# Optimization experiments

Measured on AMD Instinct MI355X. Metric: run time of the kernel, lower is better.

The kernel has to match this reference:

```python
import jax, jax.numpy as jnp
import numpy as np
from jax import lax

DN = ('NCDHW', 'OIDHW', 'NCDHW')

def _conv(x, W, strides, padding):
    return lax.conv_general_dilated(x, W, strides, padding, dimension_numbers=DN)

def setup_inputs() -> dict:
    key = jax.random.key(0)
    ks = jax.random.split(key, 7)
    B, Cin, D, H, Wd = 1, 128, 41, 128, 128
    C = 64
    feat = jax.random.normal(ks[0], (B, Cin, D, H, Wd), jnp.float32)
    mask = jax.random.uniform(ks[1], (B, 1, D, H, Wd), jnp.float32)
    def w(k, co, ci, kd, kh, kw):
        fan_in = ci * kd * kh * kw
        return jax.random.normal(k, (co, ci, kd, kh, kw), jnp.float32) * (1.0 / np.sqrt(fan_in))
    return {
        'feat': feat,
        'mask': mask,
        'W_subm0': w(ks[2], C, Cin, 3, 3, 3),
        'W_down1': w(ks[3], C, C, 3, 1, 1),
        'W_subm1a': w(ks[4], C, C, 3, 3, 3),
        'W_subm1b': w(ks[5], C, C, 3, 3, 3),
        'W_down2': w(ks[6], C, C, 3, 1, 1),
    }

def reference(feat, mask, W_subm0, W_down1, W_subm1a, W_subm1b, W_down2):
    # generate_sparse: keep only voxels where mask > 0.5 (features outside are dropped)
    m = (mask > 0.5).astype(feat.dtype)  # [B,1,D,H,W] active-site indicator
    x = feat * m
    # SubMConv3d(128->64, k=3, same) : output only at active sites -> mask the dense conv
    x = jax.nn.relu(_conv(x, W_subm0, (1, 1, 1), 'SAME') * m)
    # SparseConv3d(64->64, k=(3,1,1), stride=(2,1,1), pad=0): dense strided conv is exact
    # since x is zero at inactive sites and .dense() zero-fills inactive outputs.
    x = jax.nn.relu(_conv(x, W_down1, (2, 1, 1), 'VALID'))
    # new active set: any active input voxel in the (3,1,1)/stride-(2,1,1) window
    m = lax.reduce_window(m, 0.0, lax.max, (1, 1, 3, 1, 1), (1, 1, 2, 1, 1), 'VALID')
    # two SubMConv3d(64->64, k=3, same) on the downsampled active set
    x = jax.nn.relu(_conv(x, W_subm1a, (1, 1, 1), 'SAME') * m)
    x = jax.nn.relu(_conv(x, W_subm1b, (1, 1, 1), 'SAME') * m)
    # second strided SparseConv3d + ReLU, then .dense()
    x = jax.nn.relu(_conv(x, W_down2, (2, 1, 1), 'VALID'))
    return x  # [B, 64, 9, 128, 128]
```

## Files before the change

### kernel.cpp

```cpp
#include <hip/hip_runtime.h>

typedef __attribute__((ext_vector_type(8))) _Float16 f16x8;
typedef __attribute__((ext_vector_type(4))) float f32x4;

#define NVOX0 (41L*16384)
#define NVOX1 (20L*16384)

#define OFF_X0 0L
#define SZ_X0  (NVOX0*128*2)
#define OFF_X2 0L
#define SZ_X2  (NVOX1*64*2)
#define OFF_X3 SZ_X2
#define OFF_X4 0L
#define OFF_X1 SZ_X0
#define SZ_X1  (NVOX0*64*2)
#define OFF_M1 (OFF_X1 + SZ_X1)
#define SZ_M1  (NVOX1*4)
#define OFF_W0 (OFF_M1 + SZ_M1)
#define SZ_W0  (27L*64*128*2)
#define OFF_W1 (OFF_W0 + SZ_W0)
#define SZ_W1  (3L*64*64*2)
#define OFF_W2 (OFF_W1 + SZ_W1)
#define SZ_W2  (27L*64*64*2)
#define OFF_W3 (OFF_W2 + SZ_W2)
#define SZ_W3  (27L*64*64*2)
#define OFF_W4 (OFF_W3 + SZ_W3)
#define SZ_W4  (3L*64*64*2)

__global__ void prep_w_frag(const float* __restrict__ w, _Float16* __restrict__ o,
                            int CIN, int NK, int T) {
    int i = blockIdx.x * 256 + threadIdx.x;
    int n = T * NK * 2048;
    if (i >= n) return;
    int e = i & 7;
    int lane = (i >> 3) & 63;
    int nt = (i >> 9) & 3;
    int rest = i >> 11;
    int kc = rest % NK;
    int t = rest / NK;
    int co = nt * 16 + (lane & 15);
    int ci = kc * 32 + (lane >> 4) * 8 + e;
    o[i] = (_Float16)w[((long)co * CIN + ci) * T + t];
}

__global__ void prep_w(const float* __restrict__ w, _Float16* __restrict__ o,
                       int CO, int CI, int T) {
    int i = blockIdx.x * 256 + threadIdx.x;
    int n = CO * CI * T;
    if (i >= n) return;
    int t  = i % T;
    int ci = (i / T) % CI;
    int co = i / (T * CI);
    o[((long)t * CO + co) * CI + ci] = (_Float16)w[i];
}

__global__ void prep_m1(const float* __restrict__ mask, float* __restrict__ m1) {
    int i = blockIdx.x * 256 + threadIdx.x;
    if (i >= (int)NVOX1) return;
    int d1 = i >> 14;
    int rr = i & 16383;
    const float* p = mask + ((long)(2 * d1) << 14) + rr;
    float mx = fmaxf(p[0], fmaxf(p[16384], p[32768]));
    m1[i] = (mx > 0.5f) ? 1.0f : 0.0f;
}

__global__ __launch_bounds__(256)
void prep_x0(const float* __restrict__ feat, const float* __restrict__ mask,
             _Float16* __restrict__ x0) {
    long v = (long)blockIdx.x * 256 + threadIdx.x;
    if (v >= NVOX0) return;
    float m = (mask[v] > 0.5f) ? 1.0f : 0.0f;
    const float* fp = feat + v;
    _Float16* op = x0 + v * 128;
    #pragma unroll 2
    for (int ci0 = 0; ci0 < 128; ci0 += 8) {
        f16x8 pk;
        #pragma unroll
        for (int k = 0; k < 8; ++k)
            pk[k] = (_Float16)(fp[(long)(ci0 + k) * NVOX0] * m);
        *(f16x8*)&op[ci0] = pk;
    }
}

template<int CIN>
__global__ __launch_bounds__(128)
void subm_conv(const _Float16* __restrict__ xin,
               const float* __restrict__ mrow,
               const _Float16* __restrict__ wf,
               _Float16* __restrict__ xout,
               int D) {
    constexpr int NCH = CIN / 8;
    constexpr int NK  = CIN / 32;
    __shared__ __align__(16) _Float16 lA[130 * CIN];

    const int bid = blockIdx.x;
    const int h = ((bid & 7) << 4) | ((bid >> 3) & 15);
    const int d = bid >> 7;
    const int tid = threadIdx.x;
    const int wh = tid >> 6;
    const int lane = tid & 63;
    const int q = lane >> 4;
    const int r = lane & 15;

    f32x4 acc[4][4];
    #pragma unroll
    for (int mt = 0; mt < 4; ++mt)
        #pragma unroll
        for (int nt = 0; nt < 4; ++nt) {
            acc[mt][nt][0] = 0.f; acc[mt][nt][1] = 0.f;
            acc[mt][nt][2] = 0.f; acc[mt][nt][3] = 0.f;
        }

    for (int kd = 0; kd < 3; ++kd) {
        int id = d + kd - 1;
        if ((unsigned)id >= (unsigned)D) continue;
        for (int kh = 0; kh < 3; ++kh) {
            int ih = h + kh - 1;
            if ((unsigned)ih >= 128u) continue;
            __syncthreads();
            if (tid < 2 * NCH) {
                int slot = (tid < NCH) ? 0 : 129;
                int j = tid & (NCH - 1);
                f16x8 z = {};
                *(f16x8*)&lA[slot * CIN + j * 8] = z;
            }
            {
                const _Float16* src = xin + (((long)id * 128 + ih) * 128) * CIN;
                #pragma unroll
                for (int k = 0; k < NCH; ++k) {
                    int c = tid + k * 128;
                    int v = c / NCH;
                    int j = c & (NCH - 1);
                    int slot = v + 1;
                    f16x8 val = *(const f16x8*)&src[c * 8];
                    *(f16x8*)&lA[slot * CIN + ((j ^ (slot & 7)) << 3)] = val;
                }
            }
            __syncthreads();
            #pragma unroll
            for (int kw = 0; kw < 3; ++kw) {
                const _Float16* wb = wf + (long)((kd * 3 + kh) * 3 + kw) * NK * 2048;
                #pragma unroll
                for (int kc = 0; kc < NK; ++kc) {
                    f16x8 bf[4], af[4];
                    #pragma unroll
                    for (int nt = 0; nt < 4; ++nt)
                        bf[nt] = *(const f16x8*)&wb[((kc * 4 + nt) * 64 + lane) * 8];
                    #pragma unroll
                    for (int mt = 0; mt < 4; ++mt) {
                        int vl = wh * 64 + mt * 16 + r + kw;
                        af[mt] = *(const f16x8*)&lA[vl * CIN +
                                   ((((kc << 2) + q) ^ (vl & 7)) << 3)];
                    }
                    #pragma unroll
                    for (int mt = 0; mt < 4; ++mt)
                        #pragma unroll
                        for (int nt = 0; nt < 4; ++nt)
                            acc[mt][nt] = __builtin_amdgcn_mfma_f32_16x16x32_f16(
                                af[mt], bf[nt], acc[mt][nt], 0, 0, 0);
                }
            }
        }
    }
    long ob = (((long)d * 128 + h) * 128) * 64;
    const float* mo = mrow + ((long)d * 128 + h) * 128;
    #pragma unroll
    for (int mt = 0; mt < 4; ++mt) {
        #pragma unroll
        for (int i = 0; i < 4; ++i) {
            int v = wh * 64 + mt * 16 + q * 4 + i;
            float m = (mo[v] > 0.5f) ? 1.0f : 0.0f;
            #pragma unroll
            for (int nt = 0; nt < 4; ++nt) {
                float val = acc[mt][nt][i];
                val = val > 0.f ? val : 0.f;
                xout[ob + (long)v * 64 + nt * 16 + r] = (_Float16)(val * m);
            }
        }
    }
}

__global__ __launch_bounds__(128)
void down1_kernel(const _Float16* __restrict__ xin,
                  const _Float16* __restrict__ wt,
                  _Float16* __restrict__ xout) {
    __shared__ __align__(16) _Float16 lB[3 * 64 * 72];
    const int bid = blockIdx.x;
    const int d1 = bid >> 7;
    const int h = bid & 127;
    const int tid = threadIdx.x;
    const int wv = tid >> 6;
    const int lane = tid & 63;
    const int q = lane >> 4;
    const int r = lane & 15;

    for (int c = tid; c < 3 * 64 * 8; c += 128) {
        int row = c >> 3;
        int part = c & 7;
        *(f16x8*)&lB[row * 72 + part * 8] = *(const f16x8*)&wt[row * 64 + part * 8];
    }
    __syncthreads();

    f32x4 acc[4][4];
    #pragma unroll
    for (int mt = 0; mt < 4; ++mt)
        #pragma unroll
        for (int nt = 0; nt < 4; ++nt) {
            acc[mt][nt][0] = 0.f; acc[mt][nt][1] = 0.f;
            acc[mt][nt][2] = 0.f; acc[mt][nt][3] = 0.f;
        }

    for (int kd = 0; kd < 3; ++kd) {
        long ib = (((long)(2 * d1 + kd) * 128 + h) * 128) * 64;
        #pragma unroll
        for (int kc = 0; kc < 2; ++kc) {
            f16x8 af[4], bf[4];
            #pragma unroll
            for (int mt = 0; mt < 4; ++mt)
                af[mt] = *(const f16x8*)&xin[ib + (long)(wv * 64 + mt * 16 + r) * 64 + kc * 32 + q * 8];
            #pragma unroll
            for (int nt = 0; nt < 4; ++nt)
                bf[nt] = *(const f16x8*)&lB[(kd * 64 + nt * 16 + r) * 72 + kc * 32 + q * 8];
            #pragma unroll
            for (int mt = 0; mt < 4; ++mt)
                #pragma unroll
                for (int nt = 0; nt < 4; ++nt)
                    acc[mt][nt] = __builtin_amdgcn_mfma_f32_16x16x32_f16(
                        af[mt], bf[nt], acc[mt][nt], 0, 0, 0);
        }
    }
    long ob = (((long)d1 * 128 + h) * 128) * 64;
    #pragma unroll
    for (int mt = 0; mt < 4; ++mt)
        #pragma unroll
        for (int i = 0; i < 4; ++i) {
            int v = wv * 64 + mt * 16 + q * 4 + i;
            #pragma unroll
            for (int nt = 0; nt < 4; ++nt) {
                float val = acc[mt][nt][i];
                xout[ob + (long)v * 64 + nt * 16 + r] = (_Float16)(val > 0.f ? val : 0.f);
            }
        }
}

__global__ __launch_bounds__(128)
void down2_kernel(const _Float16* __restrict__ xin,
                  const _Float16* __restrict__ wt,
                  float* __restrict__ out) {
    __shared__ __align__(16) _Float16 lB[3 * 64 * 72];
    const int bid = blockIdx.x;
    const int d2 = bid >> 7;
    const int h = bid & 127;
    const int tid = threadIdx.x;
    const int wv = tid >> 6;
    const int lane = tid & 63;
    const int q = lane >> 4;
    const int r = lane & 15;

    for (int c = tid; c < 3 * 64 * 8; c += 128) {
        int row = c >> 3;
        int part = c & 7;
        *(f16x8*)&lB[row * 72 + part * 8] = *(const f16x8*)&wt[row * 64 + part * 8];
    }
    __syncthreads();

    f32x4 acc[4][4];
    #pragma unroll
    for (int mt = 0; mt < 4; ++mt)
        #pragma unroll
        for (int nt = 0; nt < 4; ++nt) {
            acc[mt][nt][0] = 0.f; acc[mt][nt][1] = 0.f;
            acc[mt][nt][2] = 0.f; acc[mt][nt][3] = 0.f;
        }

    for (int kd = 0; kd < 3; ++kd) {
        long ib = (((long)(2 * d2 + kd) * 128 + h) * 128) * 64;
        #pragma unroll
        for (int kc = 0; kc < 2; ++kc) {
            f16x8 wfr[4], xf[4];
            #pragma unroll
            for (int mt = 0; mt < 4; ++mt)
                wfr[mt] = *(const f16x8*)&lB[(kd * 64 + mt * 16 + r) * 72 + kc * 32 + q * 8];
            #pragma unroll
            for (int nt = 0; nt < 4; ++nt)
                xf[nt] = *(const f16x8*)&xin[ib + (long)(wv * 64 + nt * 16 + r) * 64 + kc * 32 + q * 8];
            #pragma unroll
            for (int mt = 0; mt < 4; ++mt)
                #pragma unroll
                for (int nt = 0; nt < 4; ++nt)
                    acc[mt][nt] = __builtin_amdgcn_mfma_f32_16x16x32_f16(
                        wfr[mt], xf[nt], acc[mt][nt], 0, 0, 0);
        }
    }
    #pragma unroll
    for (int mt = 0; mt < 4; ++mt)
        #pragma unroll
        for (int i = 0; i < 4; ++i) {
            int co = mt * 16 + q * 4 + i;
            #pragma unroll
            for (int nt = 0; nt < 4; ++nt) {
                int v = wv * 64 + nt * 16 + r;
                float val = acc[mt][nt][i];
                out[((long)co * 9 + d2) * 16384 + h * 128 + v] = (val > 0.f ? val : 0.f);
            }
        }
}

extern "C" void kernel_launch(void* const* d_in, const int* in_sizes, int n_in,
                              void* d_out, int out_size, void* d_ws, size_t ws_size,
                              hipStream_t stream) {
    (void)in_sizes; (void)n_in; (void)out_size; (void)ws_size;
    const float* feat = (const float*)d_in[0];
    const float* mask = (const float*)d_in[1];
    const float* w0 = (const float*)d_in[2];
    const float* w1 = (const float*)d_in[3];
    const float* w2 = (const float*)d_in[4];
    const float* w3 = (const float*)d_in[5];
    const float* w4 = (const float*)d_in[6];

    char* ws = (char*)d_ws;
    _Float16* X0  = (_Float16*)(ws + OFF_X0);
    _Float16* X1  = (_Float16*)(ws + OFF_X1);
    _Float16* X2  = (_Float16*)(ws + OFF_X2);
    _Float16* X3  = (_Float16*)(ws + OFF_X3);
    _Float16* X4  = (_Float16*)(ws + OFF_X4);
    float*    M1  = (float*)(ws + OFF_M1);
    _Float16* W0f = (_Float16*)(ws + OFF_W0);
    _Float16* W1t = (_Float16*)(ws + OFF_W1);
    _Float16* W2f = (_Float16*)(ws + OFF_W2);
    _Float16* W3f = (_Float16*)(ws + OFF_W3);
    _Float16* W4t = (_Float16*)(ws + OFF_W4);

    prep_w_frag<<<(27*4*2048 + 255) / 256, 256, 0, stream>>>(w0, W0f, 128, 4, 27);
    prep_w_frag<<<(27*2*2048 + 255) / 256, 256, 0, stream>>>(w2, W2f, 64, 2, 27);
    prep_w_frag<<<(27*2*2048 + 255) / 256, 256, 0, stream>>>(w3, W3f, 64, 2, 27);
    prep_w<<<(3*64*64 + 255) / 256, 256, 0, stream>>>(w1, W1t, 64, 64, 3);
    prep_w<<<(3*64*64 + 255) / 256, 256, 0, stream>>>(w4, W4t, 64, 64, 3);
    prep_m1<<<((int)NVOX1 + 255) / 256, 256, 0, stream>>>(mask, M1);
    prep_x0<<<(int)(NVOX0 / 256), 256, 0, stream>>>(feat, mask, X0);

    subm_conv<128><<<41 * 128, 128, 0, stream>>>(X0, mask, W0f, X1, 41);
    down1_kernel<<<20 * 128, 128, 0, stream>>>(X1, W1t, X2);
    subm_conv<64><<<20 * 128, 128, 0, stream>>>(X2, M1, W2f, X3, 20);
    subm_conv<64><<<20 * 128, 128, 0, stream>>>(X3, M1, W3f, X4, 20);
    down2_kernel<<<9 * 128, 128, 0, stream>>>(X4, W4t, (float*)d_out);
}
```

Baseline: 1.071 ms.

## Compute two depth slices per block with register-prefetched row loads

```diff
diff --git a/kernel.cpp b/kernel.cpp
--- a/kernel.cpp
+++ b/kernel.cpp
@@ -67,23 +67,24 @@
 __global__ __launch_bounds__(256)
 void prep_x0(const float* __restrict__ feat, const float* __restrict__ mask,
              _Float16* __restrict__ x0) {
-    long v = (long)blockIdx.x * 256 + threadIdx.x;
-    if (v >= NVOX0) return;
-    float m = (mask[v] > 0.5f) ? 1.0f : 0.0f;
-    const float* fp = feat + v;
-    _Float16* op = x0 + v * 128;
-    #pragma unroll 2
-    for (int ci0 = 0; ci0 < 128; ci0 += 8) {
-        f16x8 pk;
-        #pragma unroll
-        for (int k = 0; k < 8; ++k)
-            pk[k] = (_Float16)(fp[(long)(ci0 + k) * NVOX0] * m);
-        *(f16x8*)&op[ci0] = pk;
-    }
+    const int NB = (int)(NVOX0 / 16);
+    int bx = blockIdx.x;
+    int g = (bx >> 3), x = bx & 7;
+    long base = ((long)x * (NB / 8) + g) * 16;
+    int tid = threadIdx.x;
+    long vox = base + (tid >> 4);
+    int j = tid & 15;
+    float m = (mask[vox] > 0.5f) ? 1.0f : 0.0f;
+    const float* fp = feat + vox + (long)j * 8 * NVOX0;
+    f16x8 pk;
+    #pragma unroll
+    for (int k = 0; k < 8; ++k)
+        pk[k] = (_Float16)(fp[(long)k * NVOX0] * m);
+    *(f16x8*)&x0[vox * 128 + j * 8] = pk;
 }
 
 template<int CIN>
-__global__ __launch_bounds__(128)
+__global__ __launch_bounds__(256)
 void subm_conv(const _Float16* __restrict__ xin,
                const float* __restrict__ mrow,
                const _Float16* __restrict__ wf,
@@ -91,16 +92,27 @@
                int D) {
     constexpr int NCH = CIN / 8;
     constexpr int NK  = CIN / 32;
+    constexpr int NPF = 128 * NCH / 256;
     __shared__ __align__(16) _Float16 lA[130 * CIN];
 
-    const int bid = blockIdx.x;
-    const int h = ((bid & 7) << 4) | ((bid >> 3) & 15);
-    const int d = bid >> 7;
+    const int bx = blockIdx.x;
+    const int h = ((bx & 7) << 4) | (bx >> 3);
+    const int d0 = blockIdx.y * 2;
     const int tid = threadIdx.x;
-    const int wh = tid >> 6;
+    const int wv = tid >> 6;
     const int lane = tid & 63;
     const int q = lane >> 4;
     const int r = lane & 15;
+    const int out_d = d0 + (wv >> 1);
+    const int wh = wv & 1;
+    const bool vout = out_d < D;
+
+    if (tid < 2 * NCH) {
+        int slot = (tid < NCH) ? 0 : 129;
+        int j = tid & (NCH - 1);
+        f16x8 z = {};
+        *(f16x8*)&lA[slot * CIN + j * 8] = z;
+    }
 
     f32x4 acc[4][4];
     #pragma unroll
@@ -111,59 +123,79 @@
             acc[mt][nt][2] = 0.f; acc[mt][nt][3] = 0.f;
         }
 
-    for (int kd = 0; kd < 3; ++kd) {
-        int id = d + kd - 1;
-        if ((unsigned)id >= (unsigned)D) continue;
-        for (int kh = 0; kh < 3; ++kh) {
-            int ih = h + kh - 1;
-            if ((unsigned)ih >= 128u) continue;
-            __syncthreads();
-            if (tid < 2 * NCH) {
-                int slot = (tid < NCH) ? 0 : 129;
-                int j = tid & (NCH - 1);
-                f16x8 z = {};
-                *(f16x8*)&lA[slot * CIN + j * 8] = z;
-            }
-            {
-                const _Float16* src = xin + (((long)id * 128 + ih) * 128) * CIN;
-                #pragma unroll
-                for (int k = 0; k < NCH; ++k) {
-                    int c = tid + k * 128;
-                    int v = c / NCH;
-                    int j = c & (NCH - 1);
-                    int slot = v + 1;
-                    f16x8 val = *(const f16x8*)&src[c * 8];
-                    *(f16x8*)&lA[slot * CIN + ((j ^ (slot & 7)) << 3)] = val;
+    f16x8 pf[NPF];
+
+    auto rowvalid = [&](int i) -> bool {
+        int id = d0 - 1 + i / 3;
+        int ih = h - 1 + i % 3;
+        return (unsigned)id < (unsigned)D && (unsigned)ih < 128u;
+    };
+    auto do_load = [&](int i) {
+        int id = d0 - 1 + i / 3;
+        int ih = h - 1 + i % 3;
+        const _Float16* src = xin + (((long)id * 128 + ih) * 128) * CIN;
+        #pragma unroll
+        for (int k = 0; k < NPF; ++k)
+            pf[k] = *(const f16x8*)&src[(tid + k * 256) * 8];
+    };
+    auto do_write = [&]() {
+        #pragma unroll
+        for (int k = 0; k < NPF; ++k) {
+            int c = tid + k * 256;
+            int v = c / NCH;
+            int j = c & (NCH - 1);
+            int slot = v + 1;
+            *(f16x8*)&lA[slot * CIN + ((j ^ (slot & 7)) << 3)] = pf[k];
+        }
+    };
+    auto do_comp = [&](int i) {
+        int id = d0 - 1 + i / 3;
+        int ih = h - 1 + i % 3;
+        int kd = id - out_d + 1;
+        int kh = ih - h + 1;
+        if (!vout || (unsigned)kd > 2u) return;
+        #pragma unroll
+        for (int kw = 0; kw < 3; ++kw) {
+            const _Float16* wb = wf + (long)((kd * 3 + kh) * 3 + kw) * NK * 2048;
+            #pragma unroll
+            for (int kc = 0; kc < NK; ++kc) {
+                f16x8 bf[4], af[4];
+                #pragma unroll
+                for (int nt = 0; nt < 4; ++nt)
+                    bf[nt] = *(const f16x8*)&wb[((kc * 4 + nt) * 64 + lane) * 8];
+                #pragma unroll
+                for (int mt = 0; mt < 4; ++mt) {
+                    int vl = wh * 64 + mt * 16 + r + kw;
+                    af[mt] = *(const f16x8*)&lA[vl * CIN +
+                               ((((kc << 2) + q) ^ (vl & 7)) << 3)];
                 }
-            }
-            __syncthreads();
-            #pragma unroll
-            for (int kw = 0; kw < 3; ++kw) {
-                const _Float16* wb = wf + (long)((kd * 3 + kh) * 3 + kw) * NK * 2048;
-                #pragma unroll
-                for (int kc = 0; kc < NK; ++kc) {
-                    f16x8 bf[4], af[4];
+                #pragma unroll
+                for (int mt = 0; mt < 4; ++mt)
                     #pragma unroll
                     for (int nt = 0; nt < 4; ++nt)
-                        bf[nt] = *(const f16x8*)&wb[((kc * 4 + nt) * 64 + lane) * 8];
-                    #pragma unroll
-                    for (int mt = 0; mt < 4; ++mt) {
-                        int vl = wh * 64 + mt * 16 + r + kw;
-                        af[mt] = *(const f16x8*)&lA[vl * CIN +
-                                   ((((kc << 2) + q) ^ (vl & 7)) << 3)];
-                    }
-                    #pragma unroll
-                    for (int mt = 0; mt < 4; ++mt)
-                        #pragma unroll
-                        for (int nt = 0; nt < 4; ++nt)
-                            acc[mt][nt] = __builtin_amdgcn_mfma_f32_16x16x32_f16(
-                                af[mt], bf[nt], acc[mt][nt], 0, 0, 0);
-                }
+                        acc[mt][nt] = __builtin_amdgcn_mfma_f32_16x16x32_f16(
+                            af[mt], bf[nt], acc[mt][nt], 0, 0, 0);
             }
         }
-    }
-    long ob = (((long)d * 128 + h) * 128) * 64;
-    const float* mo = mrow + ((long)d * 128 + h) * 128;
+    };
+
+    int cur = 0;
+    while (cur < 12 && !rowvalid(cur)) ++cur;
+    do_load(cur);
+    while (cur < 12) {
+        int nxt = cur + 1;
+        while (nxt < 12 && !rowvalid(nxt)) ++nxt;
+        __syncthreads();
+        do_write();
+        __syncthreads();
+        if (nxt < 12) do_load(nxt);
+        do_comp(cur);
+        cur = nxt;
+    }
+
+    if (!vout) return;
+    long ob = (((long)out_d * 128 + h) * 128) * 64;
+    const float* mo = mrow + ((long)out_d * 128 + h) * 128;
     #pragma unroll
     for (int mt = 0; mt < 4; ++mt) {
         #pragma unroll
@@ -337,11 +369,11 @@
     prep_w<<<(3*64*64 + 255) / 256, 256, 0, stream>>>(w1, W1t, 64, 64, 3);
     prep_w<<<(3*64*64 + 255) / 256, 256, 0, stream>>>(w4, W4t, 64, 64, 3);
     prep_m1<<<((int)NVOX1 + 255) / 256, 256, 0, stream>>>(mask, M1);
-    prep_x0<<<(int)(NVOX0 / 256), 256, 0, stream>>>(feat, mask, X0);
-
-    subm_conv<128><<<41 * 128, 128, 0, stream>>>(X0, mask, W0f, X1, 41);
+    prep_x0<<<(int)(NVOX0 / 16), 256, 0, stream>>>(feat, mask, X0);
+
+    subm_conv<128><<<dim3(128, 21), 256, 0, stream>>>(X0, mask, W0f, X1, 41);
     down1_kernel<<<20 * 128, 128, 0, stream>>>(X1, W1t, X2);
-    subm_conv<64><<<20 * 128, 128, 0, stream>>>(X2, M1, W2f, X3, 20);
-    subm_conv<64><<<20 * 128, 128, 0, stream>>>(X3, M1, W3f, X4, 20);
+    subm_conv<64><<<dim3(128, 10), 256, 0, stream>>>(X2, M1, W2f, X3, 20);
+    subm_conv<64><<<dim3(128, 10), 256, 0, stream>>>(X3, M1, W3f, X4, 20);
     down2_kernel<<<9 * 128, 128, 0, stream>>>(X4, W4t, (float*)d_out);
 }
```

After: 1.102 ms. 1.03x slower.
